# Kernel optimization log

Hardware: AMD Instinct MI355X
Metric: run time of the kernel (lower is better)

Reference implementation:

```python
import jax, jax.numpy as jnp
import numpy as np

L = 43          # number of classes
C = L + 3       # <eps>, 'O', 'I-', + L class symbols
B = 128
T = 4096
NEG = jnp.float32(-1e30)


def setup_inputs() -> dict:
    key = jax.random.key(0)
    k1, k2, k3, k4 = jax.random.split(key, 4)
    logits = jax.random.normal(k1, (B, T, C), dtype=jnp.float32)
    log_probs = jax.nn.log_softmax(logits, axis=-1)
    input_lens = jax.random.randint(k2, (B,), T // 2, T + 1).astype(jnp.int32)
    labels = jax.random.randint(k3, (B, T), 1, C).astype(jnp.int32)  # valid (non-eps) symbols
    # den_scores parameter: one raw score per denominator arc (2L+4 arcs).
    # Layout: [0]=0->0 'O', [1:L+1]=0->0 labels, [L+1]=0->1 'I-', [L+2]=0->final,
    #         [L+3]=1->1 'I-', [L+4:2L+4]=1->0 labels.
    den_params = 0.01 * jax.random.normal(k4, (2 * L + 4,), dtype=jnp.float32)
    return {"log_probs": log_probs, "den_params": den_params,
            "input_lens": input_lens, "labels": labels}


def reference(log_probs, den_params, input_lens, labels):
    Bb, Tt, Cc = log_probs.shape
    Ll = Cc - 3
    # set_scores_stochastic_: per-source-state log-softmax of arc scores
    g0 = jax.nn.log_softmax(den_params[: Ll + 3])   # state-0 outgoing arcs
    g1 = jax.nn.log_softmax(den_params[Ll + 3:])    # state-1 outgoing arcs
    s_O, s0_lab, s_0I, s_fin = g0[0], g0[1:Ll + 1], g0[Ll + 1], g0[Ll + 2]
    s_1I, s1_lab = g1[0], g1[1:]

    mask = jnp.arange(Tt)[None, :] < input_lens[:, None]          # [B,T]

    # ---- numerator: linear FSA intersected with emissions = path score ----
    tok_lp = jnp.take_along_axis(log_probs, labels[..., None], axis=-1)[..., 0]
    num = jnp.sum(jnp.where(mask, tok_lp, 0.0), axis=1)           # [B]

    # ---- denominator: log-semiring forward DP over the 2-state topology ----
    lp_t = jnp.moveaxis(log_probs, 1, 0)    # [T,B,C]
    mask_t = jnp.moveaxis(mask, 1, 0)       # [T,B]

    def step(alpha, inputs):
        lp, m = inputs                       # lp [B,C], m [B]
        a0, a1 = alpha[:, 0], alpha[:, 1]
        lp_lab = lp[:, 3:]                   # emissions for class symbols, [B,L]
        # into state 0: 0->0 on 'O', 0->0 on each label, 1->0 on each label
        terms0 = jnp.concatenate([
            (a0 + s_O + lp[:, 1])[:, None],
            a0[:, None] + s0_lab[None, :] + lp_lab,
            a1[:, None] + s1_lab[None, :] + lp_lab,
        ], axis=1)
        n0 = jax.scipy.special.logsumexp(terms0, axis=1)
        # into state 1: 0->1 and 1->1, both on 'I-'
        terms1 = jnp.stack([a0 + s_0I + lp[:, 2], a1 + s_1I + lp[:, 2]], axis=1)
        n1 = jax.scipy.special.logsumexp(terms1, axis=1)
        new = jnp.stack([n0, n1], axis=1)
        new = jnp.where(m[:, None], new, alpha)  # frozen past each seq's length
        return new, None

    alpha0 = jnp.concatenate(
        [jnp.zeros((Bb, 1), log_probs.dtype), jnp.full((Bb, 1), NEG, log_probs.dtype)], axis=1)
    alpha, _ = jax.lax.scan(step, alpha0, (lp_t, mask_t))
    den = alpha[:, 0] + s_fin                                    # final arc 0->2 on -1

    return jnp.sum(num - den)
```

## Files before the change

### kernel.cpp

```cpp
#include <hip/hip_runtime.h>

#define BB 128
#define TT 4096
#define LL 43
#define CC 46
#define CHUNK 64
#define NC (TT / CHUNK)
#define NEGF (-1e30f)
#define L2E 1.44269504088896340736f
#define LN2 0.69314718055994530942f

__device__ __forceinline__ float fexp2(float x) { return __builtin_amdgcn_exp2f(x); }
__device__ __forceinline__ float flog2(float x) { return __builtin_amdgcn_logf(x); }
__device__ __forceinline__ float frcp(float x)  { return __builtin_amdgcn_rcpf(x); }

__device__ __forceinline__ float la2(float x, float y) {
    float mx = fmaxf(x, y), mn = fminf(x, y);
    return mx + flog2(1.0f + fexp2(mn - mx));
}

__global__ __launch_bounds__(64) void crf_chunk(
    const float* __restrict__ lp, const float* __restrict__ dp,
    const int* __restrict__ lens, const int* __restrict__ labels,
    float* __restrict__ res) {
    __shared__ float tile[CHUNK * CC];
    __shared__ float2 pp[LL + 1];
    __shared__ float sc[4];

    int b = blockIdx.y, c = blockIdx.x;
    int t0 = c * CHUNK;
    int len = lens[b];
    int lane = threadIdx.x;
    float* r = res + (b * NC + c) * 8;

    if (t0 >= len) {
        if (lane == 0) { r[0] = 0.f; r[1] = NEGF; r[2] = NEGF; r[3] = 0.f; r[4] = 0.f; }
        return;
    }

    {
        const float* gsrc = lp + (size_t)(b * TT + t0) * CC;
        #pragma unroll
        for (int s = 0; s < 11; ++s) {
            const float* g = gsrc + s * 256 + lane * 4;
            float* l = tile + s * 256;
            __builtin_amdgcn_global_load_lds(
                (const __attribute__((address_space(1))) void*)g,
                (__attribute__((address_space(3))) void*)l, 16, 0, 0);
        }
        if (lane < 32) {
            const float* g = gsrc + 11 * 256 + lane * 4;
            float* l = tile + 11 * 256;
            __builtin_amdgcn_global_load_lds(
                (const __attribute__((address_space(1))) void*)g,
                (__attribute__((address_space(3))) void*)l, 16, 0, 0);
        }
    }

    {
        float x0 = (lane < CC) ? dp[lane] : NEGF;
        float x1 = (lane < LL + 1) ? dp[CC + lane] : NEGF;
        float mx0 = x0, mx1 = x1;
        #pragma unroll
        for (int m = 1; m < 64; m <<= 1) {
            mx0 = fmaxf(mx0, __shfl_xor(mx0, m));
            mx1 = fmaxf(mx1, __shfl_xor(mx1, m));
        }
        float e0 = (lane < CC) ? fexp2(L2E * (x0 - mx0)) : 0.0f;
        float e1 = (lane < LL + 1) ? fexp2(L2E * (x1 - mx1)) : 0.0f;
        float s0 = e0, s1 = e1;
        #pragma unroll
        for (int m = 1; m < 64; m <<= 1) {
            s0 += __shfl_xor(s0, m);
            s1 += __shfl_xor(s1, m);
        }
        float r0 = frcp(s0), r1 = frcp(s1);
        float g0 = L2E * (x0 - mx0) - flog2(s0);
        float g1 = L2E * (x1 - mx1) - flog2(s1);
        if (lane >= 1 && lane <= LL) { pp[lane - 1].x = e0 * r0; pp[lane - 1].y = e1 * r1; }
        if (lane == 0) { sc[0] = e0 * r0; sc[2] = g1; }
        if (lane == LL + 1) sc[1] = g0;
        if (lane == LL + 2) sc[3] = g0;
    }

    int t = t0 + lane;
    int lab = labels[b * TT + t];
    __syncthreads();

    const float* vr = tile + lane * CC;
    float m00, m01, m10, m11, tok;
    {
        const float2* vr2 = (const float2*)vr;
        float2 c01 = vr2[0];
        float2 c23 = vr2[1];
        tok = vr[lab];
        float w1 = fexp2(L2E * c01.y);
        float v2s = L2E * c23.x;
        float dot0 = sc[0] * w1;
        float dot1 = 0.f;
        {
            float w = fexp2(L2E * c23.y);
            float2 p = pp[0];
            dot0 = fmaf(p.x, w, dot0);
            dot1 = fmaf(p.y, w, dot1);
        }
        #pragma unroll
        for (int k = 2; k <= 22; ++k) {
            float2 v = vr2[k];
            float wa = fexp2(L2E * v.x), wb = fexp2(L2E * v.y);
            float2 pa = pp[2 * k - 3], pb = pp[2 * k - 2];
            dot0 = fmaf(pa.x, wa, dot0); dot1 = fmaf(pa.y, wa, dot1);
            dot0 = fmaf(pb.x, wb, dot0); dot1 = fmaf(pb.y, wb, dot1);
        }
        m00 = dot0;
        m01 = dot1;
        m10 = fexp2(sc[1] + v2s);
        m11 = fexp2(sc[2] + v2s);
    }
    int ie = 0;
    if (t >= len) { m00 = 1.f; m01 = 0.f; m10 = 0.f; m11 = 1.f; tok = 0.f; }

    #pragma unroll
    for (int m = 1; m < 64; m <<= 1) {
        float p00 = __shfl_xor(m00, m), p01 = __shfl_xor(m01, m);
        float p10 = __shfl_xor(m10, m), p11 = __shfl_xor(m11, m);
        int   pe  = __shfl_xor(ie, m);
        float ptk = __shfl_xor(tok, m);
        bool up = (lane & m) != 0;
        float a00 = up ? m00 : p00, a01 = up ? m01 : p01;
        float a10 = up ? m10 : p10, a11 = up ? m11 : p11;
        float b00 = up ? p00 : m00, b01 = up ? p01 : m01;
        float b10 = up ? p10 : m10, b11 = up ? p11 : m11;
        float n00 = fmaf(a01, b10, a00 * b00);
        float n01 = fmaf(a01, b11, a00 * b01);
        float n10 = fmaf(a11, b10, a10 * b00);
        float n11 = fmaf(a11, b11, a10 * b01);
        float mx = fmaxf(fmaxf(n00, n01), fmaxf(n10, n11));
        unsigned bi = __float_as_uint(mx) >> 23;
        float scl = __uint_as_float((254u - bi) << 23);
        m00 = n00 * scl; m01 = n01 * scl;
        m10 = n10 * scl; m11 = n11 * scl;
        ie = ie + pe + (int)bi - 127;
        tok += ptk;
    }
    if (lane == 0) {
        float fe = (float)ie;
        r[0] = flog2(m00) + fe; r[1] = flog2(m01) + fe;
        r[2] = flog2(m10) + fe; r[3] = flog2(m11) + fe;
        r[4] = tok;
    }
}

__global__ void crf_final(const float* __restrict__ dp, const float* __restrict__ res,
                          float* __restrict__ out) {
    __shared__ float sfin2sh;
    __shared__ float part[2];
    int tid = threadIdx.x;
    if (tid < 64) {
        float x0 = (tid < CC) ? dp[tid] : NEGF;
        float mx0 = x0;
        #pragma unroll
        for (int m = 1; m < 64; m <<= 1) mx0 = fmaxf(mx0, __shfl_xor(mx0, m));
        float e0 = (tid < CC) ? fexp2(L2E * (x0 - mx0)) : 0.0f;
        float s0 = e0;
        #pragma unroll
        for (int m = 1; m < 64; m <<= 1) s0 += __shfl_xor(s0, m);
        if (tid == LL + 2) sfin2sh = L2E * (x0 - mx0) - flog2(s0);
    }
    __syncthreads();
    float a0 = 0.f, a1 = NEGF, num = 0.f;
    #pragma unroll 4
    for (int c = 0; c < NC; ++c) {
        const float* r = res + (tid * NC + c) * 8;
        float n0 = la2(r[0] + a0, r[1] + a1);
        float n1 = la2(r[2] + a0, r[3] + a1);
        a0 = n0; a1 = n1; num += r[4];
    }
    float val = num - (a0 + sfin2sh) * LN2;
    #pragma unroll
    for (int m = 1; m < 64; m <<= 1) val += __shfl_xor(val, m);
    if ((tid & 63) == 0) part[tid >> 6] = val;
    __syncthreads();
    if (tid == 0) out[0] = part[0] + part[1];
}

extern "C" void kernel_launch(void* const* d_in, const int* in_sizes, int n_in,
                              void* d_out, int out_size, void* d_ws, size_t ws_size,
                              hipStream_t stream) {
    const float* lp = (const float*)d_in[0];
    const float* dp = (const float*)d_in[1];
    const int* lens = (const int*)d_in[2];
    const int* labels = (const int*)d_in[3];
    float* out = (float*)d_out;
    float* res = (float*)d_ws;

    hipLaunchKernelGGL(crf_chunk, dim3(NC, BB), dim3(64), 0, stream,
                       lp, dp, lens, labels, res);
    hipLaunchKernelGGL(crf_final, dim3(1), dim3(128), 0, stream, dp, res, out);
}
```

Before: 150.8 us.

## Parallelize final chunk combine with wave-level 2x2 matrix product scan

```diff
diff --git a/kernel.cpp b/kernel.cpp
--- a/kernel.cpp
+++ b/kernel.cpp
@@ -13,11 +13,6 @@
 __device__ __forceinline__ float fexp2(float x) { return __builtin_amdgcn_exp2f(x); }
 __device__ __forceinline__ float flog2(float x) { return __builtin_amdgcn_logf(x); }
 __device__ __forceinline__ float frcp(float x)  { return __builtin_amdgcn_rcpf(x); }
-
-__device__ __forceinline__ float la2(float x, float y) {
-    float mx = fmaxf(x, y), mn = fminf(x, y);
-    return mx + flog2(1.0f + fexp2(mn - mx));
-}
 
 __global__ __launch_bounds__(64) void crf_chunk(
     const float* __restrict__ lp, const float* __restrict__ dp,
@@ -151,37 +146,62 @@
     }
 }
 
-__global__ void crf_final(const float* __restrict__ dp, const float* __restrict__ res,
-                          float* __restrict__ out) {
-    __shared__ float sfin2sh;
-    __shared__ float part[2];
-    int tid = threadIdx.x;
-    if (tid < 64) {
-        float x0 = (tid < CC) ? dp[tid] : NEGF;
+__global__ __launch_bounds__(256) void crf_final(
+    const float* __restrict__ dp, const float* __restrict__ res,
+    float* __restrict__ out) {
+    int wv = threadIdx.x >> 6, lane = threadIdx.x & 63;
+    int b = blockIdx.x * 4 + wv;
+
+    float sfin2;
+    {
+        float x0 = (lane < CC) ? dp[lane] : NEGF;
         float mx0 = x0;
         #pragma unroll
         for (int m = 1; m < 64; m <<= 1) mx0 = fmaxf(mx0, __shfl_xor(mx0, m));
-        float e0 = (tid < CC) ? fexp2(L2E * (x0 - mx0)) : 0.0f;
+        float e0 = (lane < CC) ? fexp2(L2E * (x0 - mx0)) : 0.0f;
         float s0 = e0;
         #pragma unroll
         for (int m = 1; m < 64; m <<= 1) s0 += __shfl_xor(s0, m);
-        if (tid == LL + 2) sfin2sh = L2E * (x0 - mx0) - flog2(s0);
-    }
-    __syncthreads();
-    float a0 = 0.f, a1 = NEGF, num = 0.f;
-    #pragma unroll 4
-    for (int c = 0; c < NC; ++c) {
-        const float* r = res + (tid * NC + c) * 8;
-        float n0 = la2(r[0] + a0, r[1] + a1);
-        float n1 = la2(r[2] + a0, r[3] + a1);
-        a0 = n0; a1 = n1; num += r[4];
-    }
-    float val = num - (a0 + sfin2sh) * LN2;
+        float g0 = L2E * (x0 - mx0) - flog2(s0);
+        sfin2 = __shfl(g0, LL + 2);
+    }
+
+    const float* r = res + (b * NC + lane) * 8;
+    float r0 = r[0], r1 = r[1], r2 = r[2], r3 = r[3], tok = r[4];
+    float rm = fmaxf(fmaxf(r0, r1), fmaxf(r2, r3));
+    int ie = (int)__builtin_floorf(rm);
+    float fe = (float)ie;
+    float m00 = fexp2(r0 - fe), m01 = fexp2(r1 - fe);
+    float m10 = fexp2(r2 - fe), m11 = fexp2(r3 - fe);
+
     #pragma unroll
-    for (int m = 1; m < 64; m <<= 1) val += __shfl_xor(val, m);
-    if ((tid & 63) == 0) part[tid >> 6] = val;
-    __syncthreads();
-    if (tid == 0) out[0] = part[0] + part[1];
+    for (int m = 1; m < 64; m <<= 1) {
+        float p00 = __shfl_xor(m00, m), p01 = __shfl_xor(m01, m);
+        float p10 = __shfl_xor(m10, m), p11 = __shfl_xor(m11, m);
+        int   pe  = __shfl_xor(ie, m);
+        float ptk = __shfl_xor(tok, m);
+        bool up = (lane & m) != 0;
+        float a00 = up ? m00 : p00, a01 = up ? m01 : p01;
+        float a10 = up ? m10 : p10, a11 = up ? m11 : p11;
+        float b00 = up ? p00 : m00, b01 = up ? p01 : m01;
+        float b10 = up ? p10 : m10, b11 = up ? p11 : m11;
+        float n00 = fmaf(a01, b10, a00 * b00);
+        float n01 = fmaf(a01, b11, a00 * b01);
+        float n10 = fmaf(a11, b10, a10 * b00);
+        float n11 = fmaf(a11, b11, a10 * b01);
+        float mx = fmaxf(fmaxf(n00, n01), fmaxf(n10, n11));
+        unsigned bi = __float_as_uint(mx) >> 23;
+        float scl = __uint_as_float((254u - bi) << 23);
+        m00 = n00 * scl; m01 = n01 * scl;
+        m10 = n10 * scl; m11 = n11 * scl;
+        ie = ie + pe + (int)bi - 127;
+        tok += ptk;
+    }
+    if (lane == 0) {
+        float den2 = flog2(m00) + (float)ie + sfin2;
+        float val = tok - den2 * LN2;
+        atomicAdd(out, val);
+    }
 }
 
 extern "C" void kernel_launch(void* const* d_in, const int* in_sizes, int n_in,
@@ -194,7 +214,8 @@
     float* out = (float*)d_out;
     float* res = (float*)d_ws;
 
+    hipMemsetAsync(out, 0, sizeof(float), stream);
     hipLaunchKernelGGL(crf_chunk, dim3(NC, BB), dim3(64), 0, stream,
                        lp, dp, lens, labels, res);
-    hipLaunchKernelGGL(crf_final, dim3(1), dim3(128), 0, stream, dp, res, out);
+    hipLaunchKernelGGL(crf_final, dim3(BB / 4), dim3(256), 0, stream, dp, res, out);
 }
```

Measured after the change: 148.1 us. About the same (-1.8%).
